# Kernel tuning notes

Hardware: AMD Instinct MI355X
Metric: run time of the kernel (lower is better)

## Reference

```python
import jax, jax.numpy as jnp
import numpy as np

N, E, D, H = 50000, 500000, 128, 8
DH = D // H  # per-head dim = int(out_dim // num_heads)
EPS_LN = 1e-5
EPS_BN = 1e-5


def _ln(x, g, b):
    m = x.mean(-1, keepdims=True)
    v = ((x - m) ** 2).mean(-1, keepdims=True)
    return (x - m) * jax.lax.rsqrt(v + EPS_LN) * g + b


def _bn(x, g, b):
    # BatchNorm1d, training-mode statistics (biased variance over the batch)
    m = x.mean(0)
    v = ((x - m) ** 2).mean(0)
    return (x - m) * jax.lax.rsqrt(v + EPS_BN) * g + b


def setup_inputs() -> dict:
    key = jax.random.key(0)
    ks = jax.random.split(key, 16)
    rn = lambda k, shape: (jax.random.normal(k, shape, jnp.float32) * 0.05)
    h = jax.random.normal(ks[0], (N, D), jnp.float32)
    src = jax.random.randint(ks[1], (E,), 0, N).astype(jnp.int32)
    # guarantee every node receives at least one message so z > 0 (no 0/0)
    dst = jnp.concatenate([jnp.arange(N, dtype=jnp.int32),
                           jax.random.randint(ks[2], (E - N,), 0, N).astype(jnp.int32)])
    return {
        "h": h, "src": src, "dst": dst,
        # per-node TransformerEncoder (seq_len == 1 subgraphs)
        "Win": rn(ks[3], (3 * D, D)), "bin": jnp.zeros((3 * D,), jnp.float32),
        "Wout": rn(ks[4], (D, D)), "bout": jnp.zeros((D,), jnp.float32),
        "Wte1": rn(ks[5], (4 * D, D)), "bte1": jnp.zeros((4 * D,), jnp.float32),
        "Wte2": rn(ks[6], (D, 4 * D)), "bte2": jnp.zeros((D,), jnp.float32),
        "ln1g": jnp.ones((D,), jnp.float32), "ln1b": jnp.zeros((D,), jnp.float32),
        "ln2g": jnp.ones((D,), jnp.float32), "ln2b": jnp.zeros((D,), jnp.float32),
        # graph multi-head attention projections (use_bias=False)
        "WQ": rn(ks[7], (D, D)), "WK": rn(ks[8], (D, D)), "WV": rn(ks[9], (D, D)),
        # node-wise FFN + batch norms
        "W1": rn(ks[10], (2 * D, D)), "b1": jnp.zeros((2 * D,), jnp.float32),
        "W2": rn(ks[11], (D, 2 * D)), "b2": jnp.zeros((D,), jnp.float32),
        "bn1g": jnp.ones((D,), jnp.float32), "bn1b": jnp.zeros((D,), jnp.float32),
        "bn2g": jnp.ones((D,), jnp.float32), "bn2b": jnp.zeros((D,), jnp.float32),
    }


def _forward(h, src, dst, Win, bin_, Wout, bout, Wte1, bte1, Wte2, bte2,
             ln1g, ln1b, ln2g, ln2b, WQ, WK, WV,
             W1, b1, W2, b2, bn1g, bn1b, bn2g, bn2b):
    # --- per-node TransformerEncoder. Each dgl.node_subgraph(g, [i]) contains
    # only the center node, so self-attention runs over a length-1 sequence:
    # softmax of a single score is 1, hence attn_out = out_proj(v).
    v = h @ Win[2 * D:].T + bin_[2 * D:]            # V slice of in_proj
    x = _ln(h + (v @ Wout.T + bout), ln1g, ln1b)
    ff = jax.nn.relu(x @ Wte1.T + bte1) @ Wte2.T + bte2
    hsub = _ln(x + ff, ln2g, ln2b)                  # [N, D]

    # --- graph multi-head attention (DGL apply_edges / send_and_recv)
    Qh = (hsub @ WQ.T).reshape(N, H, DH)
    Kh = (hsub @ WK.T).reshape(N, H, DH)
    Vh = (hsub @ WV.T).reshape(N, H, DH)
    score = (Kh[src] * Qh[dst]).sum(-1)             # [E, H]  K_src . Q_dst
    score = jnp.exp(jnp.clip(score / np.sqrt(DH), -5.0, 5.0))
    wV = jax.ops.segment_sum(Vh[src] * score[:, :, None], dst, num_segments=N)
    z = jax.ops.segment_sum(score, dst, num_segments=N)
    attn = (wV / z[:, :, None]).reshape(N, D)

    # --- residual + BN + FFN + residual + BN (dropout p=0 / eval mode)
    hh = _bn(hsub + attn, bn1g, bn1b)
    h_in2 = hh
    hh = jax.nn.relu(hh @ W1.T + b1) @ W2.T + b2
    return _bn(h_in2 + hh, bn2g, bn2b)


def reference(h, src, dst, Win, bin, Wout, bout, Wte1, bte1, Wte2, bte2,
              ln1g, ln1b, ln2g, ln2b, WQ, WK, WV,
              W1, b1, W2, b2, bn1g, bn1b, bn2g, bn2b):
    return _forward(h, src, dst, Win, bin, Wout, bout, Wte1, bte1, Wte2, bte2,
                    ln1g, ln1b, ln2g, ln2b, WQ, WK, WV,
                    W1, b1, W2, b2, bn1g, bn1b, bn2g, bn2b)
```

## Files before the change

kernel.cpp:

```cpp
#include <hip/hip_runtime.h>
#include <hip/hip_bf16.h>


#define D_ 128

typedef __attribute__((ext_vector_type(8))) short short8;
typedef __attribute__((ext_vector_type(4))) short short4v;
typedef __attribute__((ext_vector_type(4))) float f32x4;

__device__ __forceinline__ float b2f(ushort u) {
    union { uint u32; float f; } x; x.u32 = ((uint)u) << 16; return x.f;
}
__device__ __forceinline__ ushort f2b(float f) {
    union { __hip_bfloat16 h; ushort u; } v; v.h = __float2bfloat16(f); return v.u;
}

template<int AMODE, int EPI, bool RELU, bool RESF32>
__global__ __launch_bounds__(256) void gemm_bf16(
    const void* __restrict__ Aptr, const ushort* __restrict__ W,
    const float* __restrict__ bias, void* __restrict__ C,
    const float* __restrict__ bn_in, float* __restrict__ bn_out,
    const float* __restrict__ bng, const float* __restrict__ bnb,
    const void* __restrict__ resid, const ushort* __restrict__ y1res,
    const float* __restrict__ lng, const float* __restrict__ lnb,
    float invn, int n, int K, int M)
{
    __shared__ ushort Abuf[128 * 32];
    __shared__ ushort Bbuf[128 * 32];
    __shared__ float s_sh[128], t_sh[128];

    const int t    = threadIdx.x;
    const int lane = t & 63;
    const int w    = t >> 6;
    const int r0   = blockIdx.x * 128;
    const int c0   = blockIdx.y * 128;
    const int wr   = (w >> 1) * 64;
    const int wc   = (w & 1) * 64;
    const int rl   = lane & 15;
    const int kh   = lane >> 4;

    if (AMODE == 2 || EPI == 2) {
        if (t < 128) {
            float m   = bn_in[t] * invn;
            float var = bn_in[128 + t] * invn - m * m;
            float rs  = rsqrtf(var + 1e-5f);
            float s   = rs * bng[t];
            s_sh[t] = s;
            t_sh[t] = bnb[t] - m * s;
        }
        __syncthreads();
    }

    f32x4 acc[4][4] = {};

    for (int kc = 0; kc < K; kc += 32) {
        if (AMODE == 1) {
            short8 aval[2], bval[2];
            #pragma unroll
            for (int rep = 0; rep < 2; ++rep) {
                int i   = t + rep * 256;
                int row = i >> 2, ch = i & 3;
                int gr  = r0 + row;
                short8 v = {};
                if (gr < n) {
                    const float* Af = (const float*)Aptr;
                    float4 f0 = *reinterpret_cast<const float4*>(Af + (size_t)gr * K + kc + ch * 8);
                    float4 f1 = *reinterpret_cast<const float4*>(Af + (size_t)gr * K + kc + ch * 8 + 4);
                    v[0] = (short)f2b(f0.x); v[1] = (short)f2b(f0.y);
                    v[2] = (short)f2b(f0.z); v[3] = (short)f2b(f0.w);
                    v[4] = (short)f2b(f1.x); v[5] = (short)f2b(f1.y);
                    v[6] = (short)f2b(f1.z); v[7] = (short)f2b(f1.w);
                }
                aval[rep] = v;
                bval[rep] = *reinterpret_cast<const short8*>(W + (size_t)(c0 + row) * K + kc + ch * 8);
            }
            __syncthreads();
            #pragma unroll
            for (int rep = 0; rep < 2; ++rep) {
                int i   = t + rep * 256;
                int row = i >> 2, ch = i & 3;
                int sw  = ch ^ ((row >> 1) & 3);
                *reinterpret_cast<short8*>(&Abuf[row * 32 + sw * 8]) = aval[rep];
                *reinterpret_cast<short8*>(&Bbuf[row * 32 + sw * 8]) = bval[rep];
            }
            __syncthreads();
        } else {
            __syncthreads();
            #pragma unroll
            for (int rep = 0; rep < 2; ++rep) {
                int s   = t + rep * 256;
                int row = s >> 2, pos = s & 3;
                int ch  = pos ^ ((row >> 1) & 3);
                const ushort* srcA = (const ushort*)Aptr + (size_t)(r0 + row) * K + kc + ch * 8;
                const ushort* srcB = W + (size_t)(c0 + row) * K + kc + ch * 8;
                __builtin_amdgcn_global_load_lds(
                    (const __attribute__((address_space(1))) void*)srcA,
                    (__attribute__((address_space(3))) void*)&Abuf[s * 8], 16, 0, 0);
                __builtin_amdgcn_global_load_lds(
                    (const __attribute__((address_space(1))) void*)srcB,
                    (__attribute__((address_space(3))) void*)&Bbuf[s * 8], 16, 0, 0);
            }
            __syncthreads();
        }

        short8 af[4], bfr[4];
        #pragma unroll
        for (int m = 0; m < 4; ++m) {
            int row = wr + m * 16 + rl;
            af[m] = *reinterpret_cast<const short8*>(&Abuf[row * 32 + (kh ^ ((row >> 1) & 3)) * 8]);
        }
        if (AMODE == 2) {
            #pragma unroll
            for (int m = 0; m < 4; ++m) {
                short8 v = af[m];
                #pragma unroll
                for (int q = 0; q < 8; ++q) {
                    int cch = kc + kh * 8 + q;
                    v[q] = (short)f2b(fmaf(b2f((ushort)v[q]), s_sh[cch], t_sh[cch]));
                }
                af[m] = v;
            }
        }
        #pragma unroll
        for (int nn = 0; nn < 4; ++nn) {
            int col = wc + nn * 16 + rl;
            bfr[nn] = *reinterpret_cast<const short8*>(&Bbuf[col * 32 + (kh ^ ((col >> 1) & 3)) * 8]);
        }
        #pragma unroll
        for (int m = 0; m < 4; ++m)
            #pragma unroll
            for (int nn = 0; nn < 4; ++nn)
                acc[m][nn] = __builtin_amdgcn_mfma_f32_16x16x32_bf16(
                    bfr[nn], af[m], acc[m][nn], 0, 0, 0);
    }

    const int ch4 = kh * 4;

    if (EPI == 1) {
        __shared__ float lnS[128][2], lnS2[128][2];
        float4 bb[4];
        #pragma unroll
        for (int nn = 0; nn < 4; ++nn)
            bb[nn] = *reinterpret_cast<const float4*>(bias + wc + nn * 16 + ch4);
        #pragma unroll
        for (int m = 0; m < 4; ++m) {
            int r = r0 + wr + m * 16 + rl;
            float s = 0.f, s2 = 0.f;
            #pragma unroll
            for (int nn = 0; nn < 4; ++nn) {
                int c = wc + nn * 16 + ch4;
                float rv[4] = {0.f, 0.f, 0.f, 0.f};
                if (r < n) {
                    if (RESF32) {
                        float4 f = *reinterpret_cast<const float4*>((const float*)resid + (size_t)r * 128 + c);
                        rv[0] = f.x; rv[1] = f.y; rv[2] = f.z; rv[3] = f.w;
                    } else {
                        short4v f = *reinterpret_cast<const short4v*>((const ushort*)resid + (size_t)r * 128 + c);
                        rv[0] = b2f((ushort)f[0]); rv[1] = b2f((ushort)f[1]);
                        rv[2] = b2f((ushort)f[2]); rv[3] = b2f((ushort)f[3]);
                    }
                }
                float bj[4] = {bb[nn].x, bb[nn].y, bb[nn].z, bb[nn].w};
                #pragma unroll
                for (int j = 0; j < 4; ++j) {
                    float o = acc[m][nn][j] + bj[j] + rv[j];
                    acc[m][nn][j] = o;
                    s += o; s2 += o * o;
                }
            }
            s  += __shfl_xor(s, 16);  s  += __shfl_xor(s, 32);
            s2 += __shfl_xor(s2, 16); s2 += __shfl_xor(s2, 32);
            if (kh == 0) {
                lnS[wr + m * 16 + rl][w & 1]  = s;
                lnS2[wr + m * 16 + rl][w & 1] = s2;
            }
        }
        __syncthreads();
        #pragma unroll
        for (int m = 0; m < 4; ++m) {
            int rloc = wr + m * 16 + rl;
            int r = r0 + rloc;
            float S  = lnS[rloc][0] + lnS[rloc][1];
            float S2 = lnS2[rloc][0] + lnS2[rloc][1];
            float mean = S * (1.f / 128.f);
            float var  = S2 * (1.f / 128.f) - mean * mean;
            float rs   = rsqrtf(var + 1e-5f);
            if (r >= n) continue;
            #pragma unroll
            for (int nn = 0; nn < 4; ++nn) {
                int c = wc + nn * 16 + ch4;
                float4 gv = *reinterpret_cast<const float4*>(lng + c);
                float4 bv = *reinterpret_cast<const float4*>(lnb + c);
                float gj[4] = {gv.x, gv.y, gv.z, gv.w};
                float bj[4] = {bv.x, bv.y, bv.z, bv.w};
                short4v p;
                #pragma unroll
                for (int j = 0; j < 4; ++j)
                    p[j] = (short)f2b((acc[m][nn][j] - mean) * rs * gj[j] + bj[j]);
                *reinterpret_cast<short4v*>((ushort*)C + (size_t)r * 128 + c) = p;
            }
        }
        return;
    }

    if (EPI == 2) {
        __shared__ float csum[128], csum2[128];
        if (t < 128) { csum[t] = 0.f; csum2[t] = 0.f; }
        __syncthreads();
        float ps[4][4] = {};
        float ps2[4][4] = {};
        #pragma unroll
        for (int m = 0; m < 4; ++m) {
            int r = r0 + wr + m * 16 + rl;
            bool ok = r < n;
            #pragma unroll
            for (int nn = 0; nn < 4; ++nn) {
                int c = wc + nn * 16 + ch4;
                float4 bb = *reinterpret_cast<const float4*>(bias + c);
                float bj[4] = {bb.x, bb.y, bb.z, bb.w};
                short4v yv = {};
                if (ok) yv = *reinterpret_cast<const short4v*>(y1res + (size_t)r * 128 + c);
                short4v p;
                #pragma unroll
                for (int j = 0; j < 4; ++j) {
                    float o = 0.f;
                    if (ok) {
                        o = acc[m][nn][j] + bj[j]
                          + fmaf(b2f((ushort)yv[j]), s_sh[c + j], t_sh[c + j]);
                    }
                    ps[nn][j] += o; ps2[nn][j] += o * o;
                    p[j] = (short)f2b(o);
                }
                if (ok)
                    *reinterpret_cast<short4v*>((ushort*)C + (size_t)r * 128 + c) = p;
            }
        }
        #pragma unroll
        for (int nn = 0; nn < 4; ++nn)
            #pragma unroll
            for (int j = 0; j < 4; ++j) {
                float a = ps[nn][j], b = ps2[nn][j];
                #pragma unroll
                for (int o2 = 1; o2 < 16; o2 <<= 1) {
                    a += __shfl_xor(a, o2);
                    b += __shfl_xor(b, o2);
                }
                if (rl == 0) {
                    int c = wc + nn * 16 + ch4 + j;
                    atomicAdd(&csum[c], a);
                    atomicAdd(&csum2[c], b);
                }
            }
        __syncthreads();
        if (t < 128) {
            atomicAdd(bn_out + t, csum[t]);
            atomicAdd(bn_out + 128 + t, csum2[t]);
        }
        return;
    }

    #pragma unroll
    for (int m = 0; m < 4; ++m) {
        int r = r0 + wr + m * 16 + rl;
        if (r >= n) continue;
        #pragma unroll
        for (int nn = 0; nn < 4; ++nn) {
            int c = c0 + wc + nn * 16 + ch4;
            f32x4 vacc = acc[m][nn];
            float4 bb = make_float4(0.f, 0.f, 0.f, 0.f);
            if (bias) bb = *reinterpret_cast<const float4*>(bias + c);
            float o0 = vacc[0] + bb.x, o1 = vacc[1] + bb.y;
            float o2 = vacc[2] + bb.z, o3 = vacc[3] + bb.w;
            if (RELU) {
                o0 = fmaxf(o0, 0.f); o1 = fmaxf(o1, 0.f);
                o2 = fmaxf(o2, 0.f); o3 = fmaxf(o3, 0.f);
            }
            short4v p;
            p[0] = (short)f2b(o0); p[1] = (short)f2b(o1);
            p[2] = (short)f2b(o2); p[3] = (short)f2b(o3);
            *reinterpret_cast<short4v*>((ushort*)C + (size_t)r * M + c) = p;
        }
    }
}

__global__ void hist_kernel(const int* __restrict__ dst, int* __restrict__ cnt, int E_)
{
    int e = blockIdx.x * blockDim.x + threadIdx.x;
    if (e < E_) atomicAdd(cnt + dst[e], 1);
}

__global__ __launch_bounds__(256) void scan_block_kernel(
    int* __restrict__ data, int* __restrict__ bsum, int n)
{
    __shared__ int tmp[256];
    int i = blockIdx.x * 256 + threadIdx.x;
    int v = (i < n) ? data[i] : 0;
    tmp[threadIdx.x] = v;
    __syncthreads();
    #pragma unroll
    for (int o = 1; o < 256; o <<= 1) {
        int y = (threadIdx.x >= o) ? tmp[threadIdx.x - o] : 0;
        __syncthreads();
        tmp[threadIdx.x] += y;
        __syncthreads();
    }
    if (i < n) data[i] = tmp[threadIdx.x] - v;
    if (threadIdx.x == 255) bsum[blockIdx.x] = tmp[255];
}

__global__ __launch_bounds__(256) void scan_bsum_kernel(int* __restrict__ bsum, int nb)
{
    __shared__ int tmp[256];
    int v = (threadIdx.x < nb) ? bsum[threadIdx.x] : 0;
    tmp[threadIdx.x] = v;
    __syncthreads();
    #pragma unroll
    for (int o = 1; o < 256; o <<= 1) {
        int y = (threadIdx.x >= o) ? tmp[threadIdx.x - o] : 0;
        __syncthreads();
        tmp[threadIdx.x] += y;
        __syncthreads();
    }
    if (threadIdx.x < nb) bsum[threadIdx.x] = tmp[threadIdx.x] - v;
}

__global__ void add_off_kernel(int* __restrict__ data, const int* __restrict__ bsum, int n)
{
    int i = blockIdx.x * blockDim.x + threadIdx.x;
    if (i < n) data[i] += bsum[i >> 8];
}

__global__ void scatter_kernel(const int* __restrict__ src, const int* __restrict__ dst,
                               int* __restrict__ rowptr, int* __restrict__ csr_src, int E_)
{
    int e = blockIdx.x * blockDim.x + threadIdx.x;
    if (e >= E_) return;
    int pos = atomicAdd(rowptr + dst[e], 1);
    csr_src[pos] = src[e];
}

__global__ __launch_bounds__(256) void attn_agg_kernel(
    const int* __restrict__ rowptr, const int* __restrict__ csr_src,
    const ushort* __restrict__ QKV, const ushort* __restrict__ hsub,
    ushort* __restrict__ out, int n)
{
    int node = (blockIdx.x * blockDim.x + threadIdx.x) >> 6;
    if (node >= n) return;
    int lane = threadIdx.x & 63;
    int g    = lane >> 4;
    int sub  = lane & 15;
    int start = node ? rowptr[node - 1] : 0;
    int end   = rowptr[node];

    short8 q8 = *reinterpret_cast<const short8*>(QKV + (size_t)node * 384 + sub * 8);
    float q[8];
    #pragma unroll
    for (int i = 0; i < 8; ++i) q[i] = b2f((ushort)q8[i]);

    float acc[8] = {};
    float zh = 0.f;
    for (int j = start; j < end; j += 4) {
        int idx  = j + g;
        bool act = idx < end;
        int s = csr_src[act ? idx : start];
        const ushort* kvp = QKV + (size_t)s * 384;
        short8 k8 = *reinterpret_cast<const short8*>(kvp + 128 + sub * 8);
        float p = 0.f;
        #pragma unroll
        for (int i = 0; i < 8; ++i) p = fmaf(b2f((ushort)k8[i]), q[i], p);
        p += __shfl_xor(p, 1);
        float sc = act ? __expf(fminf(fmaxf(p * 0.25f, -5.f), 5.f)) : 0.f;
        short8 v8 = *reinterpret_cast<const short8*>(kvp + 256 + sub * 8);
        #pragma unroll
        for (int i = 0; i < 8; ++i) acc[i] = fmaf(sc, b2f((ushort)v8[i]), acc[i]);
        zh += sc;
    }
    #pragma unroll
    for (int i = 0; i < 8; ++i) {
        acc[i] += __shfl_xor(acc[i], 16);
        acc[i] += __shfl_xor(acc[i], 32);
    }
    zh += __shfl_xor(zh, 16);
    zh += __shfl_xor(zh, 32);

    if (g == 0) {
        short8 h8 = *reinterpret_cast<const short8*>(hsub + (size_t)node * D_ + sub * 8);
        float inv = 1.f / zh;
        short8 o;
        #pragma unroll
        for (int i = 0; i < 8; ++i)
            o[i] = (short)f2b(b2f((ushort)h8[i]) + acc[i] * inv);
        *reinterpret_cast<short8*>(out + (size_t)node * D_ + sub * 8) = o;
    }
}

__global__ __launch_bounds__(256) void bn_stats_kernel(
    const ushort* __restrict__ x, float* __restrict__ sums, int n)
{
    int c    = threadIdx.x & 127;
    int half = threadIdx.x >> 7;
    float s = 0.f, s2 = 0.f;
    for (int r = blockIdx.x * 2 + half; r < n; r += gridDim.x * 2) {
        float v = b2f(x[(size_t)r * D_ + c]);
        s += v; s2 += v * v;
    }
    __shared__ float ls[256], ls2[256];
    ls[threadIdx.x] = s; ls2[threadIdx.x] = s2;
    __syncthreads();
    if (half == 0) {
        s  += ls[threadIdx.x + 128];
        s2 += ls2[threadIdx.x + 128];
        atomicAdd(sums + c, s);
        atomicAdd(sums + 128 + c, s2);
    }
}

__global__ void bn_norm_kernel(const ushort* __restrict__ x,
                               const float* __restrict__ stats,
                               const float* __restrict__ g, const float* __restrict__ b,
                               float* __restrict__ out, float invn, int total4)
{
    int i = blockIdx.x * blockDim.x + threadIdx.x;
    if (i >= total4) return;
    int cb = (i << 2) & 127;
    short4v v = reinterpret_cast<const short4v*>(x)[i];
    float4 o;
    float r[4];
    #pragma unroll
    for (int q = 0; q < 4; ++q) {
        int c = cb + q;
        float m   = stats[c] * invn;
        float var = stats[128 + c] * invn - m * m;
        float rs  = rsqrtf(var + 1e-5f);
        r[q] = (b2f((ushort)v[q]) - m) * rs * g[c] + b[c];
    }
    o.x = r[0]; o.y = r[1]; o.z = r[2]; o.w = r[3];
    reinterpret_cast<float4*>(out)[i] = o;
}

__global__ __launch_bounds__(256) void fuse_w_kernel(
    const float* __restrict__ Win, const float* __restrict__ bin_,
    const float* __restrict__ Wout, const float* __restrict__ bout,
    ushort* __restrict__ Wf, float* __restrict__ bf)
{
    int idx = blockIdx.x * 256 + threadIdx.x;
    int i = idx >> 7, c = idx & 127;
    const float* WinV = Win + 256 * 128;
    float s = 0.f;
    for (int j = 0; j < 128; ++j)
        s = fmaf(Wout[i * 128 + j], WinV[j * 128 + c], s);
    Wf[idx] = f2b(s);
    if (c == 0) {
        float tb = bout[i];
        for (int j = 0; j < 128; ++j)
            tb = fmaf(Wout[i * 128 + j], bin_[256 + j], tb);
        bf[i] = tb;
    }
}

struct WPtrs { const float* p[7]; };

__global__ __launch_bounds__(256) void cvt_w_kernel(WPtrs wp, ushort* __restrict__ out)
{
    const int off[8] = {0, 65536, 131072, 147456, 163840, 180224, 212992, 245760};
    int e0 = (blockIdx.x * 256 + threadIdx.x) * 4;
    if (e0 >= 245760) return;
    int s = 0;
    #pragma unroll
    for (int j = 1; j < 7; ++j) if (e0 >= off[j]) s = j;
    float4 f = *reinterpret_cast<const float4*>(wp.p[s] + (e0 - off[s]));
    short4v o;
    o[0] = (short)f2b(f.x); o[1] = (short)f2b(f.y);
    o[2] = (short)f2b(f.z); o[3] = (short)f2b(f.w);
    *reinterpret_cast<short4v*>(out + e0) = o;
}

extern "C" void kernel_launch(void* const* d_in, const int* in_sizes, int n_in,
                              void* d_out, int out_size, void* d_ws, size_t ws_size,
                              hipStream_t stream)
{
    const float* h    = (const float*)d_in[0];
    const int*   src  = (const int*)d_in[1];
    const int*   dst  = (const int*)d_in[2];
    const float* Win  = (const float*)d_in[3];
    const float* bin_ = (const float*)d_in[4];
    const float* Wout = (const float*)d_in[5];
    const float* bout = (const float*)d_in[6];
    const float* Wte1 = (const float*)d_in[7];
    const float* bte1 = (const float*)d_in[8];
    const float* Wte2 = (const float*)d_in[9];
    const float* bte2 = (const float*)d_in[10];
    const float* ln1g = (const float*)d_in[11];
    const float* ln1b = (const float*)d_in[12];
    const float* ln2g = (const float*)d_in[13];
    const float* ln2b = (const float*)d_in[14];
    const float* WQ   = (const float*)d_in[15];
    const float* WK   = (const float*)d_in[16];
    const float* WV   = (const float*)d_in[17];
    const float* W1   = (const float*)d_in[18];
    const float* b1   = (const float*)d_in[19];
    const float* W2   = (const float*)d_in[20];
    const float* b2   = (const float*)d_in[21];
    const float* bn1g = (const float*)d_in[22];
    const float* bn1b = (const float*)d_in[23];
    const float* bn2g = (const float*)d_in[24];
    const float* bn2b = (const float*)d_in[25];

    const int N_ = in_sizes[0] / D_;
    const int E_ = in_sizes[1];
    const size_t S2 = (size_t)N_ * D_ / 2;

    float* ws = (float*)d_ws;
    size_t off_tail = 7 * S2;
    size_t need = (off_tail + 131072 + 128 + 512) * sizeof(float)
                + (size_t)(N_ + E_ + 256) * sizeof(int) + 4096;
    if (ws_size < need) return;

    ushort* bufA   = (ushort*)ws;
    ushort* bufB   = (ushort*)(ws + S2);
    ushort* bufC   = (ushort*)(ws + 2 * S2);
    ushort* bufD   = (ushort*)(ws + 3 * S2);
    ushort* wbf    = (ushort*)(ws + off_tail);
    float*  bfused = ws + off_tail + 131072;
    float*  stats  = bfused + 128;
    int* rowptr  = (int*)(stats + 512);
    int* csr_src = rowptr + N_;
    int* bsum    = csr_src + E_;

    const ushort* Wte1_bf = wbf;
    const ushort* Wte2_bf = wbf + 65536;
    const ushort* WQKV_bf = wbf + 131072;
    const ushort* W1_bf   = wbf + 180224;
    const ushort* W2_bf   = wbf + 212992;
    ushort*       Wf_bf   = wbf + 245760;

    dim3 blk(256);
    const int rowBlocks = (N_ + 127) / 128;
    const int totElems  = N_ * D_;
    const dim3 gRow((N_ + 3) / 4);
    const int nb = (N_ + 255) / 256;
    const float invn = 1.f / (float)N_;

    hipMemsetAsync(stats, 0, 512 * sizeof(float), stream);
    hipMemsetAsync(rowptr, 0, (size_t)N_ * sizeof(int), stream);

    hist_kernel<<<dim3((E_ + 255) / 256), blk, 0, stream>>>(dst, rowptr, E_);
    scan_block_kernel<<<dim3(nb), blk, 0, stream>>>(rowptr, bsum, N_);
    scan_bsum_kernel<<<dim3(1), blk, 0, stream>>>(bsum, nb);
    add_off_kernel<<<dim3(nb), blk, 0, stream>>>(rowptr, bsum, N_);
    scatter_kernel<<<dim3((E_ + 255) / 256), blk, 0, stream>>>(src, dst, rowptr, csr_src, E_);

    fuse_w_kernel<<<dim3(64), blk, 0, stream>>>(Win, bin_, Wout, bout, Wf_bf, bfused);
    WPtrs wp;
    wp.p[0] = Wte1; wp.p[1] = Wte2; wp.p[2] = WQ; wp.p[3] = WK; wp.p[4] = WV;
    wp.p[5] = W1;   wp.p[6] = W2;
    cvt_w_kernel<<<dim3(240), blk, 0, stream>>>(wp, wbf);

    gemm_bf16<1, 1, false, true><<<dim3(rowBlocks, 1), blk, 0, stream>>>(
        h, Wf_bf, bfused, bufA, nullptr, nullptr, nullptr, nullptr,
        h, nullptr, ln1g, ln1b, 0.f, N_, 128, 128);
    gemm_bf16<0, 0, true, false><<<dim3(rowBlocks, 4), blk, 0, stream>>>(
        bufA, Wte1_bf, bte1, bufD, nullptr, nullptr, nullptr, nullptr,
        nullptr, nullptr, nullptr, nullptr, 0.f, N_, 128, 512);
    gemm_bf16<0, 1, false, false><<<dim3(rowBlocks, 1), blk, 0, stream>>>(
        bufD, Wte2_bf, bte2, bufC, nullptr, nullptr, nullptr, nullptr,
        bufA, nullptr, ln2g, ln2b, 0.f, N_, 512, 128);

    gemm_bf16<0, 0, false, false><<<dim3(rowBlocks, 3), blk, 0, stream>>>(
        bufC, WQKV_bf, nullptr, bufD, nullptr, nullptr, nullptr, nullptr,
        nullptr, nullptr, nullptr, nullptr, 0.f, N_, 128, 384);
    attn_agg_kernel<<<gRow, blk, 0, stream>>>(
        rowptr, csr_src, bufD, bufC, bufA, N_);

    bn_stats_kernel<<<dim3(512), blk, 0, stream>>>(bufA, stats, N_);

    gemm_bf16<2, 0, true, false><<<dim3(rowBlocks, 2), blk, 0, stream>>>(
        bufA, W1_bf, b1, bufD, stats, nullptr, bn1g, bn1b,
        nullptr, nullptr, nullptr, nullptr, invn, N_, 128, 256);
    gemm_bf16<0, 2, false, false><<<dim3(rowBlocks, 1), blk, 0, stream>>>(
        bufD, W2_bf, b2, bufB, stats, stats + 256, bn1g, bn1b,
        nullptr, bufA, nullptr, nullptr, invn, N_, 256, 128);
    bn_norm_kernel<<<dim3((totElems / 4 + 255) / 256), blk, 0, stream>>>(
        bufB, stats + 256, bn2g, bn2b, (float*)d_out, invn, totElems / 4);
}
```

Baseline: 297.1 us.

## Use 512-thread GEMM blocks and 8-edge-parallel attention aggregation

The GEMM kernel now runs 8 waves per 128x128 tile, each wave computing a 32x64 sub-tile with half the accumulators, and each thread stages one 16-byte chunk instead of two. The aim is more waves per CU to hide load and sync latency, at the cost of more barrier participants and less MFMA work per wave. The attention aggregation kernel now has 8 lanes per edge, each covering one 16-wide head, so 8 edges are processed concurrently per wavefront and the per-head shuffle reduction disappears. That raises memory-level parallelism on the gathers, but each lane does 32-byte loads and adds an extra cross-slot shuffle stage in the final reduction.

```diff
diff --git a/kernel.cpp b/kernel.cpp
--- a/kernel.cpp
+++ b/kernel.cpp
@@ -16,7 +16,7 @@
 }
 
 template<int AMODE, int EPI, bool RELU, bool RESF32>
-__global__ __launch_bounds__(256) void gemm_bf16(
+__global__ __launch_bounds__(512) void gemm_bf16(
     const void* __restrict__ Aptr, const ushort* __restrict__ W,
     const float* __restrict__ bias, void* __restrict__ C,
     const float* __restrict__ bn_in, float* __restrict__ bn_out,
@@ -34,7 +34,7 @@
     const int w    = t >> 6;
     const int r0   = blockIdx.x * 128;
     const int c0   = blockIdx.y * 128;
-    const int wr   = (w >> 1) * 64;
+    const int wr   = (w >> 1) * 32;
     const int wc   = (w & 1) * 64;
     const int rl   = lane & 15;
     const int kh   = lane >> 4;
@@ -51,67 +51,52 @@
         __syncthreads();
     }
 
-    f32x4 acc[4][4] = {};
+    f32x4 acc[2][4] = {};
 
     for (int kc = 0; kc < K; kc += 32) {
+        const int row = t >> 2, pos = t & 3;
         if (AMODE == 1) {
-            short8 aval[2], bval[2];
-            #pragma unroll
-            for (int rep = 0; rep < 2; ++rep) {
-                int i   = t + rep * 256;
-                int row = i >> 2, ch = i & 3;
-                int gr  = r0 + row;
-                short8 v = {};
-                if (gr < n) {
-                    const float* Af = (const float*)Aptr;
-                    float4 f0 = *reinterpret_cast<const float4*>(Af + (size_t)gr * K + kc + ch * 8);
-                    float4 f1 = *reinterpret_cast<const float4*>(Af + (size_t)gr * K + kc + ch * 8 + 4);
-                    v[0] = (short)f2b(f0.x); v[1] = (short)f2b(f0.y);
-                    v[2] = (short)f2b(f0.z); v[3] = (short)f2b(f0.w);
-                    v[4] = (short)f2b(f1.x); v[5] = (short)f2b(f1.y);
-                    v[6] = (short)f2b(f1.z); v[7] = (short)f2b(f1.w);
-                }
-                aval[rep] = v;
-                bval[rep] = *reinterpret_cast<const short8*>(W + (size_t)(c0 + row) * K + kc + ch * 8);
-            }
+            const int ch = pos;
+            int gr = r0 + row;
+            short8 aval = {};
+            if (gr < n) {
+                const float* Af = (const float*)Aptr;
+                float4 f0 = *reinterpret_cast<const float4*>(Af + (size_t)gr * K + kc + ch * 8);
+                float4 f1 = *reinterpret_cast<const float4*>(Af + (size_t)gr * K + kc + ch * 8 + 4);
+                aval[0] = (short)f2b(f0.x); aval[1] = (short)f2b(f0.y);
+                aval[2] = (short)f2b(f0.z); aval[3] = (short)f2b(f0.w);
+                aval[4] = (short)f2b(f1.x); aval[5] = (short)f2b(f1.y);
+                aval[6] = (short)f2b(f1.z); aval[7] = (short)f2b(f1.w);
+            }
+            short8 bval = *reinterpret_cast<const short8*>(W + (size_t)(c0 + row) * K + kc + ch * 8);
             __syncthreads();
-            #pragma unroll
-            for (int rep = 0; rep < 2; ++rep) {
-                int i   = t + rep * 256;
-                int row = i >> 2, ch = i & 3;
-                int sw  = ch ^ ((row >> 1) & 3);
-                *reinterpret_cast<short8*>(&Abuf[row * 32 + sw * 8]) = aval[rep];
-                *reinterpret_cast<short8*>(&Bbuf[row * 32 + sw * 8]) = bval[rep];
-            }
+            int sw = ch ^ ((row >> 1) & 3);
+            *reinterpret_cast<short8*>(&Abuf[row * 32 + sw * 8]) = aval;
+            *reinterpret_cast<short8*>(&Bbuf[row * 32 + sw * 8]) = bval;
             __syncthreads();
         } else {
             __syncthreads();
-            #pragma unroll
-            for (int rep = 0; rep < 2; ++rep) {
-                int s   = t + rep * 256;
-                int row = s >> 2, pos = s & 3;
-                int ch  = pos ^ ((row >> 1) & 3);
-                const ushort* srcA = (const ushort*)Aptr + (size_t)(r0 + row) * K + kc + ch * 8;
-                const ushort* srcB = W + (size_t)(c0 + row) * K + kc + ch * 8;
-                __builtin_amdgcn_global_load_lds(
-                    (const __attribute__((address_space(1))) void*)srcA,
-                    (__attribute__((address_space(3))) void*)&Abuf[s * 8], 16, 0, 0);
-                __builtin_amdgcn_global_load_lds(
-                    (const __attribute__((address_space(1))) void*)srcB,
-                    (__attribute__((address_space(3))) void*)&Bbuf[s * 8], 16, 0, 0);
-            }
+            const int ch = pos ^ ((row >> 1) & 3);
+            const ushort* srcA = (const ushort*)Aptr + (size_t)(r0 + row) * K + kc + ch * 8;
+            const ushort* srcB = W + (size_t)(c0 + row) * K + kc + ch * 8;
+            __builtin_amdgcn_global_load_lds(
+                (const __attribute__((address_space(1))) void*)srcA,
+                (__attribute__((address_space(3))) void*)&Abuf[t * 8], 16, 0, 0);
+            __builtin_amdgcn_global_load_lds(
+                (const __attribute__((address_space(1))) void*)srcB,
+                (__attribute__((address_space(3))) void*)&Bbuf[t * 8], 16, 0, 0);
             __syncthreads();
         }
 
-        short8 af[4], bfr[4];
-        #pragma unroll
-        for (int m = 0; m < 4; ++m) {
-            int row = wr + m * 16 + rl;
-            af[m] = *reinterpret_cast<const short8*>(&Abuf[row * 32 + (kh ^ ((row >> 1) & 3)) * 8]);
+        short8 af[2], bfr[4];
+        #pragma unroll
+        for (int m = 0; m < 2; ++m) {
+            int rr = wr + m * 16 + rl;
+            af[m] = *reinterpret_cast<const short8*>(&Abuf[rr * 32 + (kh ^ ((rr >> 1) & 3)) * 8]);
         }
         if (AMODE == 2) {
             #pragma unroll
-            for (int m = 0; m < 4; ++m) {
+            for (int m = 0; m < 2; ++m) {
                 short8 v = af[m];
                 #pragma unroll
                 for (int q = 0; q < 8; ++q) {
@@ -127,7 +112,7 @@
             bfr[nn] = *reinterpret_cast<const short8*>(&Bbuf[col * 32 + (kh ^ ((col >> 1) & 3)) * 8]);
         }
         #pragma unroll
-        for (int m = 0; m < 4; ++m)
+        for (int m = 0; m < 2; ++m)
             #pragma unroll
             for (int nn = 0; nn < 4; ++nn)
                 acc[m][nn] = __builtin_amdgcn_mfma_f32_16x16x32_bf16(
@@ -143,7 +128,7 @@
         for (int nn = 0; nn < 4; ++nn)
             bb[nn] = *reinterpret_cast<const float4*>(bias + wc + nn * 16 + ch4);
         #pragma unroll
-        for (int m = 0; m < 4; ++m) {
+        for (int m = 0; m < 2; ++m) {
             int r = r0 + wr + m * 16 + rl;
             float s = 0.f, s2 = 0.f;
             #pragma unroll
@@ -177,7 +162,7 @@
         }
         __syncthreads();
         #pragma unroll
-        for (int m = 0; m < 4; ++m) {
+        for (int m = 0; m < 2; ++m) {
             int rloc = wr + m * 16 + rl;
             int r = r0 + rloc;
             float S  = lnS[rloc][0] + lnS[rloc][1];
@@ -210,7 +195,7 @@
         float ps[4][4] = {};
         float ps2[4][4] = {};
         #pragma unroll
-        for (int m = 0; m < 4; ++m) {
+        for (int m = 0; m < 2; ++m) {
             int r = r0 + wr + m * 16 + rl;
             bool ok = r < n;
             #pragma unroll
@@ -260,7 +245,7 @@
     }
 
     #pragma unroll
-    for (int m = 0; m < 4; ++m) {
+    for (int m = 0; m < 2; ++m) {
         int r = r0 + wr + m * 16 + rl;
         if (r >= n) continue;
         #pragma unroll
@@ -347,50 +332,67 @@
     int node = (blockIdx.x * blockDim.x + threadIdx.x) >> 6;
     if (node >= n) return;
     int lane = threadIdx.x & 63;
-    int g    = lane >> 4;
-    int sub  = lane & 15;
+    int slot = lane >> 3;
+    int hd   = lane & 7;
     int start = node ? rowptr[node - 1] : 0;
     int end   = rowptr[node];
 
-    short8 q8 = *reinterpret_cast<const short8*>(QKV + (size_t)node * 384 + sub * 8);
-    float q[8];
-    #pragma unroll
-    for (int i = 0; i < 8; ++i) q[i] = b2f((ushort)q8[i]);
-
-    float acc[8] = {};
+    const ushort* qp = QKV + (size_t)node * 384 + hd * 16;
+    short8 q0 = *reinterpret_cast<const short8*>(qp);
+    short8 q1 = *reinterpret_cast<const short8*>(qp + 8);
+    float q[16];
+    #pragma unroll
+    for (int i = 0; i < 8; ++i) { q[i] = b2f((ushort)q0[i]); q[8 + i] = b2f((ushort)q1[i]); }
+
+    float acc[16] = {};
     float zh = 0.f;
-    for (int j = start; j < end; j += 4) {
-        int idx  = j + g;
+    for (int j = start; j < end; j += 8) {
+        int idx  = j + slot;
         bool act = idx < end;
         int s = csr_src[act ? idx : start];
-        const ushort* kvp = QKV + (size_t)s * 384;
-        short8 k8 = *reinterpret_cast<const short8*>(kvp + 128 + sub * 8);
+        const ushort* kp = QKV + (size_t)s * 384 + 128 + hd * 16;
+        short8 k0 = *reinterpret_cast<const short8*>(kp);
+        short8 k1 = *reinterpret_cast<const short8*>(kp + 8);
         float p = 0.f;
         #pragma unroll
-        for (int i = 0; i < 8; ++i) p = fmaf(b2f((ushort)k8[i]), q[i], p);
-        p += __shfl_xor(p, 1);
+        for (int i = 0; i < 8; ++i) {
+            p = fmaf(b2f((ushort)k0[i]), q[i], p);
+            p = fmaf(b2f((ushort)k1[i]), q[8 + i], p);
+        }
         float sc = act ? __expf(fminf(fmaxf(p * 0.25f, -5.f), 5.f)) : 0.f;
-        short8 v8 = *reinterpret_cast<const short8*>(kvp + 256 + sub * 8);
-        #pragma unroll
-        for (int i = 0; i < 8; ++i) acc[i] = fmaf(sc, b2f((ushort)v8[i]), acc[i]);
+        short8 v0 = *reinterpret_cast<const short8*>(kp + 128);
+        short8 v1 = *reinterpret_cast<const short8*>(kp + 136);
+        #pragma unroll
+        for (int i = 0; i < 8; ++i) {
+            acc[i]     = fmaf(sc, b2f((ushort)v0[i]), acc[i]);
+            acc[8 + i] = fmaf(sc, b2f((ushort)v1[i]), acc[8 + i]);
+        }
         zh += sc;
     }
     #pragma unroll
-    for (int i = 0; i < 8; ++i) {
+    for (int i = 0; i < 16; ++i) {
+        acc[i] += __shfl_xor(acc[i], 8);
         acc[i] += __shfl_xor(acc[i], 16);
         acc[i] += __shfl_xor(acc[i], 32);
     }
+    zh += __shfl_xor(zh, 8);
     zh += __shfl_xor(zh, 16);
     zh += __shfl_xor(zh, 32);
 
-    if (g == 0) {
-        short8 h8 = *reinterpret_cast<const short8*>(hsub + (size_t)node * D_ + sub * 8);
+    if (slot == 0) {
+        const ushort* hp = hsub + (size_t)node * D_ + hd * 16;
+        short8 h0 = *reinterpret_cast<const short8*>(hp);
+        short8 h1 = *reinterpret_cast<const short8*>(hp + 8);
         float inv = 1.f / zh;
-        short8 o;
-        #pragma unroll
-        for (int i = 0; i < 8; ++i)
-            o[i] = (short)f2b(b2f((ushort)h8[i]) + acc[i] * inv);
-        *reinterpret_cast<short8*>(out + (size_t)node * D_ + sub * 8) = o;
+        short8 o0, o1;
+        #pragma unroll
+        for (int i = 0; i < 8; ++i) {
+            o0[i] = (short)f2b(b2f((ushort)h0[i]) + acc[i] * inv);
+            o1[i] = (short)f2b(b2f((ushort)h1[i]) + acc[8 + i] * inv);
+        }
+        ushort* op = out + (size_t)node * D_ + hd * 16;
+        *reinterpret_cast<short8*>(op)     = o0;
+        *reinterpret_cast<short8*>(op + 8) = o1;
     }
 }
 
@@ -535,6 +537,7 @@
     ushort*       Wf_bf   = wbf + 245760;
 
     dim3 blk(256);
+    dim3 blk512(512);
     const int rowBlocks = (N_ + 127) / 128;
     const int totElems  = N_ * D_;
     const dim3 gRow((N_ + 3) / 4);
@@ -556,17 +559,17 @@
     wp.p[5] = W1;   wp.p[6] = W2;
     cvt_w_kernel<<<dim3(240), blk, 0, stream>>>(wp, wbf);
 
-    gemm_bf16<1, 1, false, true><<<dim3(rowBlocks, 1), blk, 0, stream>>>(
+    gemm_bf16<1, 1, false, true><<<dim3(rowBlocks, 1), blk512, 0, stream>>>(
         h, Wf_bf, bfused, bufA, nullptr, nullptr, nullptr, nullptr,
         h, nullptr, ln1g, ln1b, 0.f, N_, 128, 128);
-    gemm_bf16<0, 0, true, false><<<dim3(rowBlocks, 4), blk, 0, stream>>>(
+    gemm_bf16<0, 0, true, false><<<dim3(rowBlocks, 4), blk512, 0, stream>>>(
         bufA, Wte1_bf, bte1, bufD, nullptr, nullptr, nullptr, nullptr,
         nullptr, nullptr, nullptr, nullptr, 0.f, N_, 128, 512);
-    gemm_bf16<0, 1, false, false><<<dim3(rowBlocks, 1), blk, 0, stream>>>(
+    gemm_bf16<0, 1, false, false><<<dim3(rowBlocks, 1), blk512, 0, stream>>>(
         bufD, Wte2_bf, bte2, bufC, nullptr, nullptr, nullptr, nullptr,
         bufA, nullptr, ln2g, ln2b, 0.f, N_, 512, 128);
 
-    gemm_bf16<0, 0, false, false><<<dim3(rowBlocks, 3), blk, 0, stream>>>(
+    gemm_bf16<0, 0, false, false><<<dim3(rowBlocks, 3), blk512, 0, stream>>>(
         bufC, WQKV_bf, nullptr, bufD, nullptr, nullptr, nullptr, nullptr,
         nullptr, nullptr, nullptr, nullptr, 0.f, N_, 128, 384);
     attn_agg_kernel<<<gRow, blk, 0, stream>>>(
@@ -574,10 +577,10 @@
 
     bn_stats_kernel<<<dim3(512), blk, 0, stream>>>(bufA, stats, N_);
 
-    gemm_bf16<2, 0, true, false><<<dim3(rowBlocks, 2), blk, 0, stream>>>(
+    gemm_bf16<2, 0, true, false><<<dim3(rowBlocks, 2), blk512, 0, stream>>>(
         bufA, W1_bf, b1, bufD, stats, nullptr, bn1g, bn1b,
         nullptr, nullptr, nullptr, nullptr, invn, N_, 128, 256);
-    gemm_bf16<0, 2, false, false><<<dim3(rowBlocks, 1), blk, 0, stream>>>(
+    gemm_bf16<0, 2, false, false><<<dim3(rowBlocks, 1), blk512, 0, stream>>>(
         bufD, W2_bf, b2, bufB, stats, stats + 256, bn1g, bn1b,
         nullptr, bufA, nullptr, nullptr, invn, N_, 256, 128);
     bn_norm_kernel<<<dim3((totElems / 4 + 255) / 256), blk, 0, stream>>>(
```

Result: faster. 282.9 us (-4.8%).
